# Kernel optimization log

Hardware: AMD Instinct MI355X
Metric: run time of the kernel (lower is better)

The kernel has to match this reference:

```python
import jax, jax.numpy as jnp
import numpy as np

H = 128
T_IN = 168
OUT_H = 24
B = 4096


def _lstm_cell(h, c, gates):
    # PyTorch gate order: input, forget, cell(g), output
    i, f, g, o = jnp.split(gates, 4, axis=-1)
    i = jax.nn.sigmoid(i)
    f = jax.nn.sigmoid(f)
    g = jnp.tanh(g)
    o = jax.nn.sigmoid(o)
    c_new = f * c + i * g
    h_new = o * jnp.tanh(c_new)
    return h_new, c_new


def setup_inputs() -> dict:
    key = jax.random.key(0)
    ks = jax.random.split(key, 14)
    s = 0.09  # ~1/sqrt(H) init scale, matches PyTorch LSTM default magnitude
    return {
        "x": jax.random.normal(ks[0], (B, T_IN, 1), jnp.float32),
        "enc_Wih": jax.random.normal(ks[1], (4 * H, 1), jnp.float32) * s,
        "enc_Whh": jax.random.normal(ks[2], (4 * H, H), jnp.float32) * s,
        "enc_bih": jax.random.normal(ks[3], (4 * H,), jnp.float32) * s,
        "enc_bhh": jax.random.normal(ks[4], (4 * H,), jnp.float32) * s,
        "Wa": jax.random.normal(ks[5], (H, H), jnp.float32) * s,
        "Ua": jax.random.normal(ks[6], (H, H), jnp.float32) * s,
        "va": jax.random.normal(ks[7], (H, 1), jnp.float32) * s,
        "dec_Wih": jax.random.normal(ks[8], (4 * H, 1 + H), jnp.float32) * s,
        "dec_Whh": jax.random.normal(ks[9], (4 * H, H), jnp.float32) * s,
        "dec_bih": jax.random.normal(ks[10], (4 * H,), jnp.float32) * s,
        "dec_bhh": jax.random.normal(ks[11], (4 * H,), jnp.float32) * s,
        "fc_W": jax.random.normal(ks[12], (1, H), jnp.float32) * s,
        "fc_b": jax.random.normal(ks[13], (1,), jnp.float32) * s,
    }


def reference(x, enc_Wih, enc_Whh, enc_bih, enc_bhh, Wa, Ua, va,
              dec_Wih, dec_Whh, dec_bih, dec_bhh, fc_W, fc_b):
    b = x.shape[0]
    # ---- Encoder LSTM over T_IN steps ----
    # Precompute input projection for all steps: (B, T, 4H)
    x_proj = jnp.einsum('bti,gi->btg', x, enc_Wih) + enc_bih + enc_bhh

    def enc_step(carry, xp_t):  # xp_t: (B, 4H)
        h, c = carry
        gates = xp_t + h @ enc_Whh.T
        h, c = _lstm_cell(h, c, gates)
        return (h, c), h

    h0 = jnp.zeros((b, H), x.dtype)
    c0 = jnp.zeros((b, H), x.dtype)
    (h_n, c_n), enc_hs = jax.lax.scan(enc_step, (h0, c0),
                                      jnp.swapaxes(x_proj, 0, 1))
    enc_outs = jnp.swapaxes(enc_hs, 0, 1)  # (B, T, H)

    Ue = jnp.einsum('bth,gh->btg', enc_outs, Ua)  # (B, T, H), precomputed
    v = va[:, 0]

    def dec_step(carry, _):
        h, c, din = carry  # din: (B, 1)
        energy = jnp.tanh(Ue + (h @ Wa.T)[:, None, :])       # (B, T, H)
        scores = jnp.einsum('bth,h->bt', energy, v)          # (B, T)
        attn = jax.nn.softmax(scores, axis=1)
        context = jnp.einsum('bt,bth->bh', attn, enc_outs)   # (B, H)
        inp = jnp.concatenate([din, context], axis=1)        # (B, 1+H)
        gates = inp @ dec_Wih.T + dec_bih + dec_bhh + h @ dec_Whh.T
        h2, c2 = _lstm_cell(h, c, gates)
        pred = h2 @ fc_W.T + fc_b                            # (B, 1)
        return (h2, c2, pred), pred[:, 0]

    din0 = x[:, -1, :1]  # last input value seeds the decoder
    _, preds = jax.lax.scan(dec_step, (h_n, c_n, din0), None, length=OUT_H)
    return jnp.swapaxes(preds, 0, 1)  # (B, OUT_H)
```

## Files before the change

### kernel.cpp

```cpp
#include <hip/hip_runtime.h>
#include <hip/hip_fp16.h>

#define HD 128
#define G4 512
#define TT 168
#define OUTH 24
#define NB 4096
#define RPBE 8
#define RPBD 4

typedef struct __align__(16) { __half2 a, b, c, d; } H8;

__device__ __forceinline__ float tanh_f(float x) {
  float e = __expf(2.f * x);
  return 1.f - 2.f / (e + 1.f);
}
__device__ __forceinline__ float sigm_f(float x) {
  float e = __expf(-x);
  return 1.f / (1.f + e);
}

__global__ void prep_kernel(const float* __restrict__ enc_Whh,
                            const float* __restrict__ enc_bih, const float* __restrict__ enc_bhh,
                            const float* __restrict__ Wa, const float* __restrict__ Ua,
                            const float* __restrict__ dec_Wih, const float* __restrict__ dec_Whh,
                            const float* __restrict__ dec_bih, const float* __restrict__ dec_bhh,
                            float* __restrict__ WhhT, float* __restrict__ bias_e,
                            float* __restrict__ WdT, float* __restrict__ bias_d,
                            float* __restrict__ WaT, float* __restrict__ UaT) {
  int tid = blockIdx.x * blockDim.x + threadIdx.x;
  int nt = gridDim.x * blockDim.x;
  for (int i = tid; i < HD * G4; i += nt) { int k = i / G4, g = i % G4; WhhT[i] = enc_Whh[g * HD + k]; }
  for (int i = tid; i < G4; i += nt) { bias_e[i] = enc_bih[i] + enc_bhh[i]; bias_d[i] = dec_bih[i] + dec_bhh[i]; }
  for (int i = tid; i < 257 * G4; i += nt) {
    int k = i / G4, g = i % G4;
    WdT[i] = (k < 129) ? dec_Wih[g * 129 + k] : dec_Whh[g * HD + (k - 129)];
  }
  for (int i = tid; i < HD * HD; i += nt) { int k = i / HD, j = i % HD; WaT[i] = Wa[j * HD + k]; UaT[i] = Ua[j * HD + k]; }
}

__global__ __launch_bounds__(512)
void enc_kernel(const float* __restrict__ x, const float* __restrict__ enc_Wih,
                const float* __restrict__ WhhT, const float* __restrict__ bias_e,
                __half* __restrict__ enc_f16, float* __restrict__ hn, float* __restrict__ cn) {
  __shared__ float xs[RPBE][TT];
  __shared__ float hs[HD][RPBE];
  __shared__ float cs[RPBE][HD];
  __shared__ float gs[G4][RPBE + 1];
  const int tid = threadIdx.x;
  const int g = tid;
  const int rbase = blockIdx.x * RPBE;
  for (int i = tid; i < RPBE * TT; i += 512) xs[i / TT][i % TT] = x[(size_t)rbase * TT + i];
  for (int i = tid; i < HD * RPBE; i += 512) hs[i >> 3][i & 7] = 0.f;
  for (int i = tid; i < RPBE * HD; i += 512) cs[i >> 7][i & 127] = 0.f;
  const float wih = enc_Wih[g];
  const float bias = bias_e[g];
  const int gty = g >> 7;
  const int hidx = tid & 127;
  const int rq = tid >> 7;
  __syncthreads();
  for (int t = 0; t < TT; ++t) {
    float acc[RPBE];
#pragma unroll
    for (int r = 0; r < RPBE; ++r) acc[r] = fmaf(xs[r][t], wih, bias);
#pragma unroll 4
    for (int k = 0; k < HD; ++k) {
      float w = WhhT[k * G4 + g];
      float hv[RPBE];
      *(float4*)&hv[0] = *(const float4*)&hs[k][0];
      *(float4*)&hv[4] = *(const float4*)&hs[k][4];
#pragma unroll
      for (int r = 0; r < RPBE; ++r) acc[r] = fmaf(hv[r], w, acc[r]);
    }
#pragma unroll
    for (int r = 0; r < RPBE; ++r) gs[g][r] = (gty == 2) ? tanh_f(acc[r]) : sigm_f(acc[r]);
    __syncthreads();
#pragma unroll
    for (int rr = 0; rr < 2; ++rr) {
      int r = rq * 2 + rr;
      float iv = gs[hidx][r], fv = gs[128 + hidx][r], gv = gs[256 + hidx][r], ov = gs[384 + hidx][r];
      float c = fmaf(fv, cs[r][hidx], iv * gv);
      cs[r][hidx] = c;
      float h = ov * tanh_f(c);
      hs[hidx][r] = h;
      enc_f16[((size_t)(rbase + r) * TT + t) * HD + hidx] = __float2half(h);
    }
    __syncthreads();
  }
#pragma unroll
  for (int rr = 0; rr < 2; ++rr) {
    int r = rq * 2 + rr;
    hn[(size_t)(rbase + r) * HD + hidx] = hs[hidx][r];
    cn[(size_t)(rbase + r) * HD + hidx] = cs[r][hidx];
  }
}

__global__ __launch_bounds__(256)
void ue_kernel(const __half* __restrict__ enc_f16, const float* __restrict__ UaT,
               __half* __restrict__ Ue) {
  __shared__ float es[HD][68];
  const int tid = threadIdx.x;
  const int j = tid & 127, rh = tid >> 7;
  const size_t nbase = (size_t)blockIdx.x * 64;
  for (int i = tid; i < 64 * 64; i += 256) {
    int row = i >> 6, k2 = i & 63;
    __half2 hv = ((const __half2*)enc_f16)[(nbase + row) * 64 + k2];
    float2 f = __half22float2(hv);
    es[2 * k2][row] = f.x;
    es[2 * k2 + 1][row] = f.y;
  }
  __syncthreads();
  float acc[32];
#pragma unroll
  for (int r = 0; r < 32; ++r) acc[r] = 0.f;
  const int rb = rh * 32;
  for (int k = 0; k < HD; ++k) {
    float w = UaT[k * HD + j];
    float ev[32];
#pragma unroll
    for (int q = 0; q < 8; ++q) *(float4*)&ev[q * 4] = *(const float4*)&es[k][rb + q * 4];
#pragma unroll
    for (int r = 0; r < 32; ++r) acc[r] = fmaf(ev[r], w, acc[r]);
  }
#pragma unroll
  for (int r = 0; r < 32; ++r) Ue[(nbase + rb + r) * HD + j] = __float2half(acc[r]);
}

__global__ __launch_bounds__(512)
void dec_kernel(const float* __restrict__ x, const __half* __restrict__ enc_f16,
                const __half* __restrict__ Ue,
                const float* __restrict__ hn, const float* __restrict__ cn,
                const float* __restrict__ WaT, const float* __restrict__ va,
                const float* __restrict__ WdT, const float* __restrict__ bias_d,
                const float* __restrict__ fc_W, const float* __restrict__ fc_b,
                float* __restrict__ out) {
  __shared__ float inp[257][8];
  __shared__ float cs[RPBD][HD];
  __shared__ float ppart[RPBD][2];
  __shared__ float upool[G4 * 5];
  float (*qsh)[HD] = (float(*)[HD])upool;
  float (*ssh)[TT] = (float(*)[TT])(upool + RPBD * HD);
  float (*cpart)[RPBD][HD] = (float(*)[RPBD][HD])(upool + RPBD * HD + RPBD * TT);
  float (*gsh)[5] = (float(*)[5])upool;

  const int tid = threadIdx.x;
  const int rbase = blockIdx.x * RPBD;
  const int jq = tid & 3, tl = tid >> 2;
  const int hidx = tid & 127, rq = tid >> 7;
  const int g = tid;
  const int gty = g >> 7;
  const float biasd = bias_d[g];
  const float fcw = fc_W[hidx];
  const float fcb = fc_b[0];
  float vr[32];
#pragma unroll
  for (int i = 0; i < 32; ++i) vr[i] = va[jq * 32 + i];

  {
    int r = tid >> 7, k = tid & 127;
    inp[129 + k][r] = hn[(size_t)(rbase + r) * HD + k];
    cs[r][k] = cn[(size_t)(rbase + r) * HD + k];
  }
  if (tid < RPBD) inp[0][tid] = x[(size_t)(rbase + tid) * TT + (TT - 1)];
  __syncthreads();

  for (int s = 0; s < OUTH; ++s) {
    {
      float qa = 0.f;
      for (int k = 0; k < HD; ++k) qa = fmaf(inp[129 + k][rq], WaT[k * HD + hidx], qa);
      qsh[rq][hidx] = qa;
    }
    __syncthreads();
#pragma unroll
    for (int r = 0; r < RPBD; ++r) {
      float qr[32];
#pragma unroll
      for (int q4 = 0; q4 < 8; ++q4) *(float4*)&qr[q4 * 4] = *(const float4*)&qsh[r][jq * 32 + q4 * 4];
      const __half* Uep = Ue + ((size_t)(rbase + r) * TT) * HD + jq * 32;
#pragma unroll
      for (int i2 = 0; i2 < 2; ++i2) {
        int t = tl + i2 * 128;
        if (t < TT) {
          const H8* up = (const H8*)(Uep + (size_t)t * HD);
          float sp = 0.f;
#pragma unroll
          for (int c8 = 0; c8 < 4; ++c8) {
            H8 hv = up[c8];
            float2 f0 = __half22float2(hv.a);
            float2 f1 = __half22float2(hv.b);
            float2 f2 = __half22float2(hv.c);
            float2 f3 = __half22float2(hv.d);
            int b0 = c8 * 8;
            sp = fmaf(tanh_f(f0.x + qr[b0 + 0]), vr[b0 + 0], sp);
            sp = fmaf(tanh_f(f0.y + qr[b0 + 1]), vr[b0 + 1], sp);
            sp = fmaf(tanh_f(f1.x + qr[b0 + 2]), vr[b0 + 2], sp);
            sp = fmaf(tanh_f(f1.y + qr[b0 + 3]), vr[b0 + 3], sp);
            sp = fmaf(tanh_f(f2.x + qr[b0 + 4]), vr[b0 + 4], sp);
            sp = fmaf(tanh_f(f2.y + qr[b0 + 5]), vr[b0 + 5], sp);
            sp = fmaf(tanh_f(f3.x + qr[b0 + 6]), vr[b0 + 6], sp);
            sp = fmaf(tanh_f(f3.y + qr[b0 + 7]), vr[b0 + 7], sp);
          }
          sp += __shfl_xor(sp, 1);
          sp += __shfl_xor(sp, 2);
          if (jq == 0) ssh[r][t] = sp;
        }
      }
    }
    __syncthreads();
    if (tid < 128) {
      int r = tid >> 5, l = tid & 31;
      float m = -1e30f;
      for (int t = l; t < TT; t += 32) m = fmaxf(m, ssh[r][t]);
#pragma unroll
      for (int o = 1; o < 32; o <<= 1) m = fmaxf(m, __shfl_xor(m, o, 32));
      float se = 0.f;
      for (int t = l; t < TT; t += 32) { float e = __expf(ssh[r][t] - m); ssh[r][t] = e; se += e; }
#pragma unroll
      for (int o = 1; o < 32; o <<= 1) se += __shfl_xor(se, o, 32);
      float inv = 1.f / se;
      for (int t = l; t < TT; t += 32) ssh[r][t] *= inv;
    }
    __syncthreads();
    {
      int jp = tid & 63, r = (tid >> 6) & 3, th = tid >> 8;
      int t0 = th * 84, t1 = t0 + 84;
      const __half2* ep = (const __half2*)(enc_f16 + ((size_t)(rbase + r) * TT) * HD) + jp;
      float c0 = 0.f, c1 = 0.f;
#pragma unroll 4
      for (int t = t0; t < t1; ++t) {
        float a = ssh[r][t];
        float2 ef = __half22float2(ep[(size_t)t * 64]);
        c0 = fmaf(a, ef.x, c0);
        c1 = fmaf(a, ef.y, c1);
      }
      cpart[th][r][2 * jp] = c0;
      cpart[th][r][2 * jp + 1] = c1;
    }
    __syncthreads();
    {
      int k = tid & 127, r = tid >> 7;
      inp[1 + k][r] = cpart[0][r][k] + cpart[1][r][k];
    }
    __syncthreads();
    {
      float a0 = biasd, a1 = biasd, a2 = biasd, a3 = biasd;
#pragma unroll 4
      for (int k = 0; k < 257; ++k) {
        float w = WdT[k * G4 + g];
        float4 iv = *(const float4*)&inp[k][0];
        a0 = fmaf(iv.x, w, a0);
        a1 = fmaf(iv.y, w, a1);
        a2 = fmaf(iv.z, w, a2);
        a3 = fmaf(iv.w, w, a3);
      }
      if (gty == 2) {
        gsh[g][0] = tanh_f(a0); gsh[g][1] = tanh_f(a1); gsh[g][2] = tanh_f(a2); gsh[g][3] = tanh_f(a3);
      } else {
        gsh[g][0] = sigm_f(a0); gsh[g][1] = sigm_f(a1); gsh[g][2] = sigm_f(a2); gsh[g][3] = sigm_f(a3);
      }
    }
    __syncthreads();
    {
      float iv = gsh[hidx][rq], fv = gsh[128 + hidx][rq], gv = gsh[256 + hidx][rq], ov = gsh[384 + hidx][rq];
      float c = fmaf(fv, cs[rq][hidx], iv * gv);
      cs[rq][hidx] = c;
      float h2 = ov * tanh_f(c);
      inp[129 + hidx][rq] = h2;
      float sv = h2 * fcw;
#pragma unroll
      for (int o = 1; o < 64; o <<= 1) sv += __shfl_xor(sv, o);
      if ((tid & 63) == 0) ppart[rq][(tid >> 6) & 1] = sv;
    }
    __syncthreads();
    if (tid < RPBD) {
      float pred = ppart[tid][0] + ppart[tid][1] + fcb;
      out[(size_t)(rbase + tid) * OUTH + s] = pred;
      inp[0][tid] = pred;
    }
    __syncthreads();
  }
}

extern "C" void kernel_launch(void* const* d_in, const int* in_sizes, int n_in,
                              void* d_out, int out_size, void* d_ws, size_t ws_size,
                              hipStream_t stream) {
  const float* x       = (const float*)d_in[0];
  const float* enc_Wih = (const float*)d_in[1];
  const float* enc_Whh = (const float*)d_in[2];
  const float* enc_bih = (const float*)d_in[3];
  const float* enc_bhh = (const float*)d_in[4];
  const float* Wa      = (const float*)d_in[5];
  const float* Ua      = (const float*)d_in[6];
  const float* va      = (const float*)d_in[7];
  const float* dec_Wih = (const float*)d_in[8];
  const float* dec_Whh = (const float*)d_in[9];
  const float* dec_bih = (const float*)d_in[10];
  const float* dec_bhh = (const float*)d_in[11];
  const float* fc_W    = (const float*)d_in[12];
  const float* fc_b    = (const float*)d_in[13];
  float* out = (float*)d_out;

  char* ws = (char*)d_ws;
  size_t off = 0;
  float* WhhT = (float*)(ws + off); off += (size_t)HD * G4 * 4;
  float* be   = (float*)(ws + off); off += (size_t)G4 * 4;
  float* WdT  = (float*)(ws + off); off += (size_t)257 * G4 * 4;
  float* bd   = (float*)(ws + off); off += (size_t)G4 * 4;
  float* WaT  = (float*)(ws + off); off += (size_t)HD * HD * 4;
  float* UaT  = (float*)(ws + off); off += (size_t)HD * HD * 4;
  float* hn   = (float*)(ws + off); off += (size_t)NB * HD * 4;
  float* cn   = (float*)(ws + off); off += (size_t)NB * HD * 4;
  const size_t rowB = (size_t)TT * HD * 2;
  size_t avail = (ws_size > off) ? ws_size - off : 0;
  int CE, CD;
  if (avail >= 2 * (size_t)NB * rowB) {
    CE = NB; CD = NB;
  } else if (avail >= (size_t)NB * rowB + 16 * rowB) {
    CE = NB;
    CD = NB;
    while (CD > 16 && (size_t)NB * rowB + (size_t)CD * rowB > avail) CD >>= 1;
  } else {
    int c = NB;
    while (c > 16 && 2 * (size_t)c * rowB > avail) c >>= 1;
    if (2 * (size_t)c * rowB > avail) return;
    CE = CD = c;
  }
  __half* encb = (__half*)(ws + off);
  __half* ueb  = (__half*)(ws + off + (size_t)CE * rowB);

  prep_kernel<<<dim3(64), dim3(256), 0, stream>>>(enc_Whh, enc_bih, enc_bhh, Wa, Ua,
      dec_Wih, dec_Whh, dec_bih, dec_bhh, WhhT, be, WdT, bd, WaT, UaT);

  if (CE == NB) {
    enc_kernel<<<dim3(NB / RPBE), dim3(512), 0, stream>>>(x, enc_Wih, WhhT, be, encb, hn, cn);
    for (int c0 = 0; c0 < NB; c0 += CD) {
      const __half* ec = encb + (size_t)c0 * TT * HD;
      ue_kernel<<<dim3(CD * TT / 64), dim3(256), 0, stream>>>(ec, UaT, ueb);
      dec_kernel<<<dim3(CD / RPBD), dim3(512), 0, stream>>>(x + (size_t)c0 * TT, ec, ueb,
          hn + (size_t)c0 * HD, cn + (size_t)c0 * HD, WaT, va, WdT, bd, fc_W, fc_b,
          out + (size_t)c0 * OUTH);
    }
  } else {
    for (int c0 = 0; c0 < NB; c0 += CE) {
      enc_kernel<<<dim3(CE / RPBE), dim3(512), 0, stream>>>(x + (size_t)c0 * TT, enc_Wih, WhhT, be,
          encb, hn + (size_t)c0 * HD, cn + (size_t)c0 * HD);
      ue_kernel<<<dim3(CE * TT / 64), dim3(256), 0, stream>>>(encb, UaT, ueb);
      dec_kernel<<<dim3(CE / RPBD), dim3(512), 0, stream>>>(x + (size_t)c0 * TT, encb, ueb,
          hn + (size_t)c0 * HD, cn + (size_t)c0 * HD, WaT, va, WdT, bd, fc_W, fc_b,
          out + (size_t)c0 * OUTH);
    }
  }
}
```

Baseline: 8.765 ms.

## Halve decoder rows per block and split context reduction four ways

```diff
diff --git a/kernel.cpp b/kernel.cpp
--- a/kernel.cpp
+++ b/kernel.cpp
@@ -7,7 +7,7 @@
 #define OUTH 24
 #define NB 4096
 #define RPBE 8
-#define RPBD 4
+#define RPBD 2
 
 typedef struct __align__(16) { __half2 a, b, c, d; } H8;
 
@@ -134,14 +134,13 @@
                 const float* __restrict__ WdT, const float* __restrict__ bias_d,
                 const float* __restrict__ fc_W, const float* __restrict__ fc_b,
                 float* __restrict__ out) {
-  __shared__ float inp[257][8];
-  __shared__ float cs[RPBD][HD];
+  __shared__ float inp[257][4];
+  __shared__ float cs2[RPBD][HD];
   __shared__ float ppart[RPBD][2];
-  __shared__ float upool[G4 * 5];
-  float (*qsh)[HD] = (float(*)[HD])upool;
-  float (*ssh)[TT] = (float(*)[TT])(upool + RPBD * HD);
-  float (*cpart)[RPBD][HD] = (float(*)[RPBD][HD])(upool + RPBD * HD + RPBD * TT);
-  float (*gsh)[5] = (float(*)[5])upool;
+  __shared__ float qsh[RPBD][HD];
+  __shared__ float ssh[RPBD][TT];
+  __shared__ float cpart[4][RPBD][HD];
+  __shared__ float gsh[G4][3];
 
   const int tid = threadIdx.x;
   const int rbase = blockIdx.x * RPBD;
@@ -156,16 +155,16 @@
 #pragma unroll
   for (int i = 0; i < 32; ++i) vr[i] = va[jq * 32 + i];
 
-  {
+  if (tid < RPBD * HD) {
     int r = tid >> 7, k = tid & 127;
     inp[129 + k][r] = hn[(size_t)(rbase + r) * HD + k];
-    cs[r][k] = cn[(size_t)(rbase + r) * HD + k];
+    cs2[r][k] = cn[(size_t)(rbase + r) * HD + k];
   }
   if (tid < RPBD) inp[0][tid] = x[(size_t)(rbase + tid) * TT + (TT - 1)];
   __syncthreads();
 
   for (int s = 0; s < OUTH; ++s) {
-    {
+    if (rq < RPBD) {
       float qa = 0.f;
       for (int k = 0; k < HD; ++k) qa = fmaf(inp[129 + k][rq], WaT[k * HD + hidx], qa);
       qsh[rq][hidx] = qa;
@@ -207,7 +206,7 @@
       }
     }
     __syncthreads();
-    if (tid < 128) {
+    if (tid < RPBD * 32) {
       int r = tid >> 5, l = tid & 31;
       float m = -1e30f;
       for (int t = l; t < TT; t += 32) m = fmaxf(m, ssh[r][t]);
@@ -222,8 +221,8 @@
     }
     __syncthreads();
     {
-      int jp = tid & 63, r = (tid >> 6) & 3, th = tid >> 8;
-      int t0 = th * 84, t1 = t0 + 84;
+      int jp = tid & 63, r = (tid >> 6) & 1, th = tid >> 7;
+      int t0 = th * 42, t1 = t0 + 42;
       const __half2* ep = (const __half2*)(enc_f16 + ((size_t)(rbase + r) * TT) * HD) + jp;
       float c0 = 0.f, c1 = 0.f;
 #pragma unroll 4
@@ -237,33 +236,28 @@
       cpart[th][r][2 * jp + 1] = c1;
     }
     __syncthreads();
+    if (tid < RPBD * HD) {
+      int k = tid & 127, r = tid >> 7;
+      inp[1 + k][r] = (cpart[0][r][k] + cpart[1][r][k]) + (cpart[2][r][k] + cpart[3][r][k]);
+    }
+    __syncthreads();
     {
-      int k = tid & 127, r = tid >> 7;
-      inp[1 + k][r] = cpart[0][r][k] + cpart[1][r][k];
-    }
-    __syncthreads();
-    {
-      float a0 = biasd, a1 = biasd, a2 = biasd, a3 = biasd;
+      float a0 = biasd, a1 = biasd;
 #pragma unroll 4
       for (int k = 0; k < 257; ++k) {
         float w = WdT[k * G4 + g];
-        float4 iv = *(const float4*)&inp[k][0];
+        float2 iv = *(const float2*)&inp[k][0];
         a0 = fmaf(iv.x, w, a0);
         a1 = fmaf(iv.y, w, a1);
-        a2 = fmaf(iv.z, w, a2);
-        a3 = fmaf(iv.w, w, a3);
       }
-      if (gty == 2) {
-        gsh[g][0] = tanh_f(a0); gsh[g][1] = tanh_f(a1); gsh[g][2] = tanh_f(a2); gsh[g][3] = tanh_f(a3);
-      } else {
-        gsh[g][0] = sigm_f(a0); gsh[g][1] = sigm_f(a1); gsh[g][2] = sigm_f(a2); gsh[g][3] = sigm_f(a3);
-      }
-    }
-    __syncthreads();
-    {
+      if (gty == 2) { gsh[g][0] = tanh_f(a0); gsh[g][1] = tanh_f(a1); }
+      else          { gsh[g][0] = sigm_f(a0); gsh[g][1] = sigm_f(a1); }
+    }
+    __syncthreads();
+    if (rq < RPBD) {
       float iv = gsh[hidx][rq], fv = gsh[128 + hidx][rq], gv = gsh[256 + hidx][rq], ov = gsh[384 + hidx][rq];
-      float c = fmaf(fv, cs[rq][hidx], iv * gv);
-      cs[rq][hidx] = c;
+      float c = fmaf(fv, cs2[rq][hidx], iv * gv);
+      cs2[rq][hidx] = c;
       float h2 = ov * tanh_f(c);
       inp[129 + hidx][rq] = h2;
       float sv = h2 * fcw;
@@ -315,12 +309,14 @@
   int CE, CD;
   if (avail >= 2 * (size_t)NB * rowB) {
     CE = NB; CD = NB;
-  } else if (avail >= (size_t)NB * rowB + 16 * rowB) {
-    CE = NB;
-    CD = NB;
-    while (CD > 16 && (size_t)NB * rowB + (size_t)CD * rowB > avail) CD >>= 1;
+  } else if (avail >= (size_t)NB * rowB + (size_t)2048 * rowB) {
+    CE = NB; CD = 2048;
+  } else if (avail >= (size_t)NB * rowB + (size_t)1024 * rowB) {
+    CE = NB; CD = 1024;
+  } else if (avail >= (size_t)NB * rowB + (size_t)512 * rowB) {
+    CE = NB; CD = 512;
   } else {
-    int c = NB;
+    int c = 2048;
     while (c > 16 && 2 * (size_t)c * rowB > avail) c >>= 1;
     if (2 * (size_t)c * rowB > avail) return;
     CE = CD = c;
```

After: 13.34 ms. +52.2%, slower.
